# Performance work log

Measured on AMD Instinct MI355X. Metric: run time of the kernel, lower is better.

## Reference

```python
import jax, jax.numpy as jnp
import numpy as np

N_NODES = 100000
N_EDGES = 640000
N_FEAT = 128


def setup_inputs() -> dict:
    key = jax.random.key(0)
    k1, k2, k3, k4 = jax.random.split(key, 4)
    x = jax.random.normal(k1, (N_NODES, N_FEAT), dtype=jnp.float32)
    edge_index = jax.random.randint(k2, (2, N_EDGES), 0, N_NODES, dtype=jnp.int32)
    # Glorot-ish init for weights
    W_conv = jax.random.normal(k3, (N_FEAT, N_FEAT), dtype=jnp.float32) / np.sqrt(N_FEAT)
    b_conv = jnp.zeros((N_FEAT,), dtype=jnp.float32)
    W_lin = jax.random.normal(k4, (1, N_FEAT), dtype=jnp.float32) / np.sqrt(N_FEAT)
    b_lin = jnp.zeros((1,), dtype=jnp.float32)
    return {"x": x, "edge_index": edge_index, "W_conv": W_conv,
            "b_conv": b_conv, "W_lin": W_lin, "b_lin": b_lin}


def gcn_conv(x, edge_index, W, b):
    # PyG GCNConv: add self-loops, symmetric normalization D^-1/2 (A+I) D^-1/2,
    # linear transform first (no bias in lin), bias added after aggregation.
    N = x.shape[0]
    loop = jnp.arange(N, dtype=edge_index.dtype)
    src = jnp.concatenate([edge_index[0], loop])  # [E+N]
    dst = jnp.concatenate([edge_index[1], loop])  # [E+N]
    deg = jax.ops.segment_sum(jnp.ones_like(dst, dtype=x.dtype), dst, num_segments=N)
    dinv = jnp.where(deg > 0, jax.lax.rsqrt(deg), 0.0)
    norm = dinv[src] * dinv[dst]                   # [E+N]
    xw = x @ W.T                                   # [N, F]
    msg = xw[src] * norm[:, None]                  # [E+N, F] gather + scale
    agg = jax.ops.segment_sum(msg, dst, num_segments=N)  # scatter-add
    return agg + b


def reference(x, edge_index, W_conv, b_conv, W_lin, b_lin):
    h = jax.nn.relu(gcn_conv(x, edge_index, W_conv, b_conv))
    out = jax.nn.sigmoid(h @ W_lin.T + b_lin)
    return (out, h)
```

## Files before the change

### kernel.cpp

```cpp
#include <hip/hip_runtime.h>
#include <hip/hip_bf16.h>

#define NN 100000
#define NE 640000
#define NF 128
#define CAP 32
#define ECAP 36
#define LDW 136
#define XBLK 12500

typedef short bf16x8 __attribute__((ext_vector_type(8)));
typedef float f32x4  __attribute__((ext_vector_type(4)));

__device__ __forceinline__ unsigned short f2bf(float f) {
    union { float f; unsigned int i; } v; v.f = f;
    unsigned int x = v.i;
    return (unsigned short)((x + 0x7FFFu + ((x >> 16) & 1u)) >> 16);
}


__global__ void k_zero(int* __restrict__ fill) {
    int i = blockIdx.x * blockDim.x + threadIdx.x;
    if (i < NN) fill[i] = 0;
}

__global__ void k_fill(const int* __restrict__ src, const int* __restrict__ dst,
                       int* __restrict__ fill, int* __restrict__ esrc) {
    int e = blockIdx.x * blockDim.x + threadIdx.x;
    if (e >= NE) return;
    int s = src[e], d = dst[e];
    int pos = atomicAdd(&fill[d], 1);
    if (pos < CAP) esrc[d * CAP + pos] = s;
}

__global__ void k_prep(const float* __restrict__ x, const int* __restrict__ fill,
                       const float* __restrict__ W,
                       unsigned short* __restrict__ xs,
                       unsigned short* __restrict__ wb) {
    int b = blockIdx.x;
    if (b < XBLK) {
        int t = b * 256 + threadIdx.x;
        int node = t >> 5, fc = (t & 31) * 4;
        float dv = rsqrtf((float)(fill[node] + 1));
        float4 xv = *(const float4*)(x + (long)node * NF + fc);
        ushort4 u;
        u.x = f2bf(xv.x * dv); u.y = f2bf(xv.y * dv);
        u.z = f2bf(xv.z * dv); u.w = f2bf(xv.w * dv);
        *(ushort4*)(xs + (long)node * NF + fc) = u;
    } else {
        int t = (b - XBLK) * 256 + threadIdx.x;
        int idx = t * 4;
        float4 wv = *(const float4*)(W + idx);
        ushort4 u;
        u.x = f2bf(wv.x); u.y = f2bf(wv.y); u.z = f2bf(wv.z); u.w = f2bf(wv.w);
        *(ushort4*)(wb + idx) = u;
    }
}

__device__ __forceinline__ void acc_row(float* acc, int4 u) {
    acc[0] += __int_as_float((unsigned)u.x << 16);
    acc[1] += __int_as_float(u.x & 0xffff0000);
    acc[2] += __int_as_float((unsigned)u.y << 16);
    acc[3] += __int_as_float(u.y & 0xffff0000);
    acc[4] += __int_as_float((unsigned)u.z << 16);
    acc[5] += __int_as_float(u.z & 0xffff0000);
    acc[6] += __int_as_float((unsigned)u.w << 16);
    acc[7] += __int_as_float(u.w & 0xffff0000);
}

__launch_bounds__(256, 4)
__global__ void k_fused(const unsigned short* __restrict__ xs,
                        const int* __restrict__ fill,
                        const int* __restrict__ esrc,
                        const unsigned short* __restrict__ wb,
                        const float* __restrict__ bconv,
                        const float* __restrict__ wlin,
                        const float* __restrict__ blin,
                        float* __restrict__ out,
                        float* __restrict__ hout) {
    __shared__ unsigned short lds_a[32 * LDW];
    __shared__ int lds_e[32 * ECAP];
    __shared__ float lds_dv[32];
    __shared__ int lds_dg[32];
    __shared__ float sh_head[2][32];
    int t = threadIdx.x;
    int row0 = blockIdx.x * 32;

    {
        int r = t >> 3, col = (t & 7) * 4;
        *(int4*)(lds_e + r * ECAP + col) =
            *(const int4*)(esrc + (long)(row0 + r) * CAP + col);
    }
    if (t < 32) {
        int dg = fill[row0 + t];
        lds_dv[t] = rsqrtf((float)(dg + 1));
        lds_dg[t] = (dg > CAP) ? CAP : dg;
    }
    __syncthreads();

    {
        int lane = t & 15, slot = t >> 4;
        int fc = lane * 8;
        for (int m = 0; m < 2; ++m) {
            int r = m * 16 + slot;
            int node = row0 + r;
            float dv = lds_dv[r];
            int degc = lds_dg[r];
            const int* ep = lds_e + r * ECAP;

            float acc[8];
            {
                int4 us = *(const int4*)(xs + (long)node * NF + fc);
                acc[0] = __int_as_float((unsigned)us.x << 16);
                acc[1] = __int_as_float(us.x & 0xffff0000);
                acc[2] = __int_as_float((unsigned)us.y << 16);
                acc[3] = __int_as_float(us.y & 0xffff0000);
                acc[4] = __int_as_float((unsigned)us.z << 16);
                acc[5] = __int_as_float(us.z & 0xffff0000);
                acc[6] = __int_as_float((unsigned)us.w << 16);
                acc[7] = __int_as_float(us.w & 0xffff0000);
            }

            int j = 0;
            for (; j + 8 <= degc; j += 8) {
                int4 ea = *(const int4*)(ep + j);
                int4 eb = *(const int4*)(ep + j + 4);
                int4 v0 = *(const int4*)(xs + (long)ea.x * NF + fc);
                int4 v1 = *(const int4*)(xs + (long)ea.y * NF + fc);
                int4 v2 = *(const int4*)(xs + (long)ea.z * NF + fc);
                int4 v3 = *(const int4*)(xs + (long)ea.w * NF + fc);
                int4 v4 = *(const int4*)(xs + (long)eb.x * NF + fc);
                int4 v5 = *(const int4*)(xs + (long)eb.y * NF + fc);
                int4 v6 = *(const int4*)(xs + (long)eb.z * NF + fc);
                int4 v7 = *(const int4*)(xs + (long)eb.w * NF + fc);
                acc_row(acc, v0); acc_row(acc, v1);
                acc_row(acc, v2); acc_row(acc, v3);
                acc_row(acc, v4); acc_row(acc, v5);
                acc_row(acc, v6); acc_row(acc, v7);
            }
            if (j + 4 <= degc) {
                int4 e4 = *(const int4*)(ep + j);
                int4 v0 = *(const int4*)(xs + (long)e4.x * NF + fc);
                int4 v1 = *(const int4*)(xs + (long)e4.y * NF + fc);
                int4 v2 = *(const int4*)(xs + (long)e4.z * NF + fc);
                int4 v3 = *(const int4*)(xs + (long)e4.w * NF + fc);
                acc_row(acc, v0); acc_row(acc, v1);
                acc_row(acc, v2); acc_row(acc, v3);
                j += 4;
            }
            for (; j < degc; ++j) {
                int s = ep[j];
                int4 u = *(const int4*)(xs + (long)s * NF + fc);
                acc_row(acc, u);
            }

            int4 st;
            st.x = (unsigned)f2bf(acc[0] * dv) | ((unsigned)f2bf(acc[1] * dv) << 16);
            st.y = (unsigned)f2bf(acc[2] * dv) | ((unsigned)f2bf(acc[3] * dv) << 16);
            st.z = (unsigned)f2bf(acc[4] * dv) | ((unsigned)f2bf(acc[5] * dv) << 16);
            st.w = (unsigned)f2bf(acc[6] * dv) | ((unsigned)f2bf(acc[7] * dv) << 16);
            *(int4*)(lds_a + r * LDW + fc) = st;
        }
    }
    __syncthreads();

    int w = t >> 6, lane = t & 63;
    int quad = lane >> 4, nr = lane & 15;
    int mrow = (w >> 1) * 16;
    int ncol0 = (w & 1) * 64;
    int kq = quad * 8;

    f32x4 acc4[4];
#pragma unroll
    for (int nt = 0; nt < 4; ++nt) acc4[nt] = (f32x4){0.f, 0.f, 0.f, 0.f};

#pragma unroll
    for (int ks = 0; ks < 4; ++ks) {
        bf16x8 af = *(const bf16x8*)(lds_a + (mrow + nr) * LDW + ks * 32 + kq);
#pragma unroll
        for (int nt = 0; nt < 4; ++nt) {
            bf16x8 bf = *(const bf16x8*)(wb + (ncol0 + nt * 16 + nr) * NF + ks * 32 + kq);
            acc4[nt] = __builtin_amdgcn_mfma_f32_16x16x32_bf16(af, bf, acc4[nt], 0, 0, 0);
        }
    }

    float bcv[4], wlv[4];
#pragma unroll
    for (int nt = 0; nt < 4; ++nt) {
        int col = ncol0 + nt * 16 + nr;
        bcv[nt] = bconv[col];
        wlv[nt] = wlin[col];
    }
    float p[4] = {0.f, 0.f, 0.f, 0.f};
#pragma unroll
    for (int nt = 0; nt < 4; ++nt) {
        int col = ncol0 + nt * 16 + nr;
#pragma unroll
        for (int r = 0; r < 4; ++r) {
            float h = fmaxf(acc4[nt][r] + bcv[nt], 0.0f);
            int row = row0 + mrow + quad * 4 + r;
            hout[(long)row * NF + col] = h;
            p[r] += h * wlv[nt];
        }
    }
#pragma unroll
    for (int r = 0; r < 4; ++r) {
#pragma unroll
        for (int off = 1; off <= 8; off <<= 1)
            p[r] += __shfl_xor(p[r], off, 64);
        if (nr == 0) sh_head[w & 1][mrow + quad * 4 + r] = p[r];
    }
    __syncthreads();
    if (t < 32) {
        float z = sh_head[0][t] + sh_head[1][t] + blin[0];
        out[row0 + t] = 1.0f / (1.0f + expf(-z));
    }
}

extern "C" void kernel_launch(void* const* d_in, const int* in_sizes, int n_in,
                              void* d_out, int out_size, void* d_ws, size_t ws_size,
                              hipStream_t stream) {
    const float* x     = (const float*)d_in[0];
    const int*   ei    = (const int*)d_in[1];
    const float* Wc    = (const float*)d_in[2];
    const float* bconv = (const float*)d_in[3];
    const float* wlin  = (const float*)d_in[4];
    const float* blin  = (const float*)d_in[5];
    const int* src = ei;
    const int* dst = ei + NE;

    float* out  = (float*)d_out;
    float* hout = out + NN;

    int*            esrc = (int*)d_ws;
    unsigned short* xs   = (unsigned short*)(esrc + (size_t)NN * CAP);
    unsigned short* wb   = xs + (size_t)NN * NF;
    int*            fill = (int*)(wb + NF * NF);

    k_zero <<<(NN + 255) / 256, 256, 0, stream>>>(fill);
    k_fill <<<(NE + 255) / 256, 256, 0, stream>>>(src, dst, fill, esrc);
    k_prep <<<XBLK + 16, 256, 0, stream>>>(x, fill, Wc, xs, wb);
    k_fused<<<NN / 32, 256, 0, stream>>>(xs, fill, esrc, wb,
                                         bconv, wlin, blin, out, hout);
}
```

Baseline: 196.2 us.

## Merge edge fill and bf16 conversion into one kernel, apply source norm in gather

Before, x was converted to bf16 pre-scaled by the source node's inverse sqrt degree, which meant conversion had to wait for the edge-count pass. Now x is converted unscaled, so edge bucketing, x conversion and W conversion run as independent block ranges of a single launch, removing one launch and the dependency between them. The source-degree scaling moves into the gather loop: each neighbour's fill count is loaded, rsqrt is taken, and an FMA replaces the plain add. This adds a scattered 4-byte load and an rsqrt per edge in the hot aggregation kernel, and the unscaled bf16 values change rounding slightly.

```diff
diff --git a/kernel.cpp b/kernel.cpp
--- a/kernel.cpp
+++ b/kernel.cpp
@@ -7,7 +7,9 @@
 #define CAP 32
 #define ECAP 36
 #define LDW 136
-#define XBLK 12500
+#define EBLK 2500
+#define XBLK 6250
+#define WBLK 8
 
 typedef short bf16x8 __attribute__((ext_vector_type(8)));
 typedef float f32x4  __attribute__((ext_vector_type(4)));
@@ -18,54 +20,57 @@
     return (unsigned short)((x + 0x7FFFu + ((x >> 16) & 1u)) >> 16);
 }
 
-
 __global__ void k_zero(int* __restrict__ fill) {
     int i = blockIdx.x * blockDim.x + threadIdx.x;
-    if (i < NN) fill[i] = 0;
-}
-
-__global__ void k_fill(const int* __restrict__ src, const int* __restrict__ dst,
-                       int* __restrict__ fill, int* __restrict__ esrc) {
-    int e = blockIdx.x * blockDim.x + threadIdx.x;
-    if (e >= NE) return;
-    int s = src[e], d = dst[e];
-    int pos = atomicAdd(&fill[d], 1);
-    if (pos < CAP) esrc[d * CAP + pos] = s;
-}
-
-__global__ void k_prep(const float* __restrict__ x, const int* __restrict__ fill,
-                       const float* __restrict__ W,
-                       unsigned short* __restrict__ xs,
-                       unsigned short* __restrict__ wb) {
+    if (i < NN / 4) *(int4*)(fill + i * 4) = (int4){0, 0, 0, 0};
+}
+
+__global__ void k_build(const float* __restrict__ x, const float* __restrict__ W,
+                        const int* __restrict__ src, const int* __restrict__ dst,
+                        int* __restrict__ fill, int* __restrict__ esrc,
+                        unsigned short* __restrict__ xs,
+                        unsigned short* __restrict__ wb) {
     int b = blockIdx.x;
-    if (b < XBLK) {
-        int t = b * 256 + threadIdx.x;
-        int node = t >> 5, fc = (t & 31) * 4;
-        float dv = rsqrtf((float)(fill[node] + 1));
-        float4 xv = *(const float4*)(x + (long)node * NF + fc);
-        ushort4 u;
-        u.x = f2bf(xv.x * dv); u.y = f2bf(xv.y * dv);
-        u.z = f2bf(xv.z * dv); u.w = f2bf(xv.w * dv);
-        *(ushort4*)(xs + (long)node * NF + fc) = u;
+    if (b < EBLK) {
+        int e = b * 256 + threadIdx.x;
+        int s = src[e], d = dst[e];
+        int pos = atomicAdd(&fill[d], 1);
+        if (pos < CAP) esrc[(long)d * CAP + pos] = s;
+    } else if (b < EBLK + XBLK) {
+        int t = (b - EBLK) * 256 + threadIdx.x;
+        int node = t >> 4, fc = (t & 15) * 8;
+        const float* xp = x + (long)node * NF + fc;
+        float4 a = *(const float4*)(xp);
+        float4 c = *(const float4*)(xp + 4);
+        int4 u;
+        u.x = (unsigned)f2bf(a.x) | ((unsigned)f2bf(a.y) << 16);
+        u.y = (unsigned)f2bf(a.z) | ((unsigned)f2bf(a.w) << 16);
+        u.z = (unsigned)f2bf(c.x) | ((unsigned)f2bf(c.y) << 16);
+        u.w = (unsigned)f2bf(c.z) | ((unsigned)f2bf(c.w) << 16);
+        *(int4*)(xs + (long)node * NF + fc) = u;
     } else {
-        int t = (b - XBLK) * 256 + threadIdx.x;
-        int idx = t * 4;
-        float4 wv = *(const float4*)(W + idx);
-        ushort4 u;
-        u.x = f2bf(wv.x); u.y = f2bf(wv.y); u.z = f2bf(wv.z); u.w = f2bf(wv.w);
-        *(ushort4*)(wb + idx) = u;
-    }
-}
-
-__device__ __forceinline__ void acc_row(float* acc, int4 u) {
-    acc[0] += __int_as_float((unsigned)u.x << 16);
-    acc[1] += __int_as_float(u.x & 0xffff0000);
-    acc[2] += __int_as_float((unsigned)u.y << 16);
-    acc[3] += __int_as_float(u.y & 0xffff0000);
-    acc[4] += __int_as_float((unsigned)u.z << 16);
-    acc[5] += __int_as_float(u.z & 0xffff0000);
-    acc[6] += __int_as_float((unsigned)u.w << 16);
-    acc[7] += __int_as_float(u.w & 0xffff0000);
+        int t = (b - EBLK - XBLK) * 256 + threadIdx.x;
+        int idx = t * 8;
+        float4 a = *(const float4*)(W + idx);
+        float4 c = *(const float4*)(W + idx + 4);
+        int4 u;
+        u.x = (unsigned)f2bf(a.x) | ((unsigned)f2bf(a.y) << 16);
+        u.y = (unsigned)f2bf(a.z) | ((unsigned)f2bf(a.w) << 16);
+        u.z = (unsigned)f2bf(c.x) | ((unsigned)f2bf(c.y) << 16);
+        u.w = (unsigned)f2bf(c.z) | ((unsigned)f2bf(c.w) << 16);
+        *(int4*)(wb + idx) = u;
+    }
+}
+
+__device__ __forceinline__ void acc_row_s(float* acc, int4 u, float s) {
+    acc[0] = fmaf(s, __int_as_float((unsigned)u.x << 16), acc[0]);
+    acc[1] = fmaf(s, __int_as_float(u.x & 0xffff0000), acc[1]);
+    acc[2] = fmaf(s, __int_as_float((unsigned)u.y << 16), acc[2]);
+    acc[3] = fmaf(s, __int_as_float(u.y & 0xffff0000), acc[3]);
+    acc[4] = fmaf(s, __int_as_float((unsigned)u.z << 16), acc[4]);
+    acc[5] = fmaf(s, __int_as_float(u.z & 0xffff0000), acc[5]);
+    acc[6] = fmaf(s, __int_as_float((unsigned)u.w << 16), acc[6]);
+    acc[7] = fmaf(s, __int_as_float(u.w & 0xffff0000), acc[7]);
 }
 
 __launch_bounds__(256, 4)
@@ -111,20 +116,24 @@
             float acc[8];
             {
                 int4 us = *(const int4*)(xs + (long)node * NF + fc);
-                acc[0] = __int_as_float((unsigned)us.x << 16);
-                acc[1] = __int_as_float(us.x & 0xffff0000);
-                acc[2] = __int_as_float((unsigned)us.y << 16);
-                acc[3] = __int_as_float(us.y & 0xffff0000);
-                acc[4] = __int_as_float((unsigned)us.z << 16);
-                acc[5] = __int_as_float(us.z & 0xffff0000);
-                acc[6] = __int_as_float((unsigned)us.w << 16);
-                acc[7] = __int_as_float(us.w & 0xffff0000);
+                acc[0] = dv * __int_as_float((unsigned)us.x << 16);
+                acc[1] = dv * __int_as_float(us.x & 0xffff0000);
+                acc[2] = dv * __int_as_float((unsigned)us.y << 16);
+                acc[3] = dv * __int_as_float(us.y & 0xffff0000);
+                acc[4] = dv * __int_as_float((unsigned)us.z << 16);
+                acc[5] = dv * __int_as_float(us.z & 0xffff0000);
+                acc[6] = dv * __int_as_float((unsigned)us.w << 16);
+                acc[7] = dv * __int_as_float(us.w & 0xffff0000);
             }
 
             int j = 0;
             for (; j + 8 <= degc; j += 8) {
                 int4 ea = *(const int4*)(ep + j);
                 int4 eb = *(const int4*)(ep + j + 4);
+                int f0 = fill[ea.x], f1 = fill[ea.y];
+                int f2 = fill[ea.z], f3 = fill[ea.w];
+                int f4 = fill[eb.x], f5 = fill[eb.y];
+                int f6 = fill[eb.z], f7 = fill[eb.w];
                 int4 v0 = *(const int4*)(xs + (long)ea.x * NF + fc);
                 int4 v1 = *(const int4*)(xs + (long)ea.y * NF + fc);
                 int4 v2 = *(const int4*)(xs + (long)ea.z * NF + fc);
@@ -133,25 +142,34 @@
                 int4 v5 = *(const int4*)(xs + (long)eb.y * NF + fc);
                 int4 v6 = *(const int4*)(xs + (long)eb.z * NF + fc);
                 int4 v7 = *(const int4*)(xs + (long)eb.w * NF + fc);
-                acc_row(acc, v0); acc_row(acc, v1);
-                acc_row(acc, v2); acc_row(acc, v3);
-                acc_row(acc, v4); acc_row(acc, v5);
-                acc_row(acc, v6); acc_row(acc, v7);
+                acc_row_s(acc, v0, rsqrtf((float)(f0 + 1)));
+                acc_row_s(acc, v1, rsqrtf((float)(f1 + 1)));
+                acc_row_s(acc, v2, rsqrtf((float)(f2 + 1)));
+                acc_row_s(acc, v3, rsqrtf((float)(f3 + 1)));
+                acc_row_s(acc, v4, rsqrtf((float)(f4 + 1)));
+                acc_row_s(acc, v5, rsqrtf((float)(f5 + 1)));
+                acc_row_s(acc, v6, rsqrtf((float)(f6 + 1)));
+                acc_row_s(acc, v7, rsqrtf((float)(f7 + 1)));
             }
             if (j + 4 <= degc) {
                 int4 e4 = *(const int4*)(ep + j);
+                int f0 = fill[e4.x], f1 = fill[e4.y];
+                int f2 = fill[e4.z], f3 = fill[e4.w];
                 int4 v0 = *(const int4*)(xs + (long)e4.x * NF + fc);
                 int4 v1 = *(const int4*)(xs + (long)e4.y * NF + fc);
                 int4 v2 = *(const int4*)(xs + (long)e4.z * NF + fc);
                 int4 v3 = *(const int4*)(xs + (long)e4.w * NF + fc);
-                acc_row(acc, v0); acc_row(acc, v1);
-                acc_row(acc, v2); acc_row(acc, v3);
+                acc_row_s(acc, v0, rsqrtf((float)(f0 + 1)));
+                acc_row_s(acc, v1, rsqrtf((float)(f1 + 1)));
+                acc_row_s(acc, v2, rsqrtf((float)(f2 + 1)));
+                acc_row_s(acc, v3, rsqrtf((float)(f3 + 1)));
                 j += 4;
             }
             for (; j < degc; ++j) {
                 int s = ep[j];
+                int fdeg = fill[s];
                 int4 u = *(const int4*)(xs + (long)s * NF + fc);
-                acc_row(acc, u);
+                acc_row_s(acc, u, rsqrtf((float)(fdeg + 1)));
             }
 
             int4 st;
@@ -237,9 +255,9 @@
     unsigned short* wb   = xs + (size_t)NN * NF;
     int*            fill = (int*)(wb + NF * NF);
 
-    k_zero <<<(NN + 255) / 256, 256, 0, stream>>>(fill);
-    k_fill <<<(NE + 255) / 256, 256, 0, stream>>>(src, dst, fill, esrc);
-    k_prep <<<XBLK + 16, 256, 0, stream>>>(x, fill, Wc, xs, wb);
+    k_zero <<<(NN / 4 + 255) / 256, 256, 0, stream>>>(fill);
+    k_build<<<EBLK + XBLK + WBLK, 256, 0, stream>>>(x, Wc, src, dst,
+                                                    fill, esrc, xs, wb);
     k_fused<<<NN / 32, 256, 0, stream>>>(xs, fill, esrc, wb,
                                          bconv, wlin, blin, out, hout);
 }
```

New measurement: 195.3 us. Within noise of the previous version (-0.5%).
